# Performance work log

Hardware: AMD Instinct MI355X
Metric: run time of the kernel (lower is better)

Reference implementation:

```python
import jax, jax.numpy as jnp
import numpy as np

D = 1024
H = 16
HD = D // H
S = 1024
FF = 4 * D
EPS = 1e-5


def _layernorm(x, g, b):
    mu = jnp.mean(x, axis=-1, keepdims=True)
    var = jnp.var(x, axis=-1, keepdims=True)
    return (x - mu) * jax.lax.rsqrt(var + EPS) * g + b


def _mha(q_in, k_in, v_in, wq, bq, wk, bk, wv, bv, wo, bo, causal):
    # weights stored [in, out]; per-head torch Linears concatenated == one [D, D] projection
    def split(x, w, bias):
        y = x @ w + bias                      # [B, S, D]
        B, L, _ = y.shape
        return y.reshape(B, L, H, HD).transpose(0, 2, 1, 3)  # [B, H, L, HD]

    q = split(q_in, wq, bq)
    k = split(k_in, wk, bk)
    v = split(v_in, wv, bv)
    scores = jnp.einsum('bhqd,bhkd->bhqk', q, k) / np.sqrt(HD).astype(np.float32)
    if causal:
        mask = jnp.triu(jnp.ones((scores.shape[-2], scores.shape[-1]), dtype=bool), 1)
        scores = jnp.where(mask, -jnp.inf, scores)
    attn = jax.nn.softmax(scores, axis=-1)
    rep = jnp.einsum('bhqk,bhkd->bhqd', attn, v)
    B, _, L, _ = rep.shape
    rep = rep.transpose(0, 2, 1, 3).reshape(B, L, D)
    return rep @ wo + bo


def setup_inputs() -> dict:
    key = jax.random.key(0)
    ks = jax.random.split(key, 24)
    sc = 0.02
    d = {}
    d['decoder'] = jax.random.normal(ks[0], (8, S, D), dtype=jnp.float32)
    d['encoder'] = jax.random.normal(ks[1], (8, S, D), dtype=jnp.float32)
    names = ['sa_wq', 'sa_wk', 'sa_wv', 'sa_wo', 'ca_wq', 'ca_wk', 'ca_wv', 'ca_wo']
    for i, n in enumerate(names):
        d[n] = jax.random.normal(ks[2 + i], (D, D), dtype=jnp.float32) * sc
        d[n.replace('w', 'b')] = jnp.zeros((D,), dtype=jnp.float32)
    for i in range(1, 4):
        d[f'ln{i}_g'] = jnp.ones((D,), dtype=jnp.float32)
        d[f'ln{i}_b'] = jnp.zeros((D,), dtype=jnp.float32)
    d['ffn_w1'] = jax.random.normal(ks[10], (D, FF), dtype=jnp.float32) * sc
    d['ffn_b1'] = jnp.zeros((FF,), dtype=jnp.float32)
    d['ffn_w2'] = jax.random.normal(ks[11], (FF, D), dtype=jnp.float32) * sc
    d['ffn_b2'] = jnp.zeros((D,), dtype=jnp.float32)
    return d


def reference(decoder, encoder,
              sa_wq, sa_bq, sa_wk, sa_bk, sa_wv, sa_bv, sa_wo, sa_bo,
              ca_wq, ca_bq, ca_wk, ca_bk, ca_wv, ca_bv, ca_wo, ca_bo,
              ln1_g, ln1_b, ln2_g, ln2_b, ln3_g, ln3_b,
              ffn_w1, ffn_b1, ffn_w2, ffn_b2):
    # masked self-attention; NOTE: residual uses the *normalized* embeddings (faithful to source)
    x = _layernorm(decoder, ln1_g, ln1_b)
    x = x + _mha(x, x, x, sa_wq, sa_bq, sa_wk, sa_bk, sa_wv, sa_bv, sa_wo, sa_bo, causal=True)
    # cross-attention to (unnormalized) encoder output
    y = _layernorm(x, ln2_g, ln2_b)
    y = y + _mha(y, encoder, encoder, ca_wq, ca_bq, ca_wk, ca_bk, ca_wv, ca_bv, ca_wo, ca_bo, causal=False)
    # GELU FFN
    z = _layernorm(y, ln3_g, ln3_b)
    h = jax.nn.gelu(z @ ffn_w1 + ffn_b1, approximate=False)
    out = z + (h @ ffn_w2 + ffn_b2)
    return out
```

## Files before the change

kernel.cpp:

```cpp
#include <hip/hip_runtime.h>
#include <math.h>

typedef unsigned short u16;
typedef unsigned int u32;

typedef __attribute__((ext_vector_type(8))) short short8;
typedef __attribute__((ext_vector_type(4))) float floatx4;
typedef __attribute__((ext_vector_type(4))) unsigned short ushort4v;

#define DD 1024
#define HH 16
#define HD 64
#define SS 1024
#define BBATCH 8
#define FFDIM 4096
#define MM (BBATCH*SS)

__device__ __forceinline__ float bf2f(u16 v){ u32 x = ((u32)v)<<16; return __builtin_bit_cast(float, x); }
__device__ __forceinline__ u16 f2bf(float f){
  u32 x = __builtin_bit_cast(u32, f);
  u32 r = (x + 0x7fffu + ((x>>16)&1u)) >> 16;
  return (u16)r;
}

__device__ __forceinline__ void gload_lds16(const void* g, void* l){
  __builtin_amdgcn_global_load_lds((const __attribute__((address_space(1))) void*)g,
                                   (__attribute__((address_space(3))) void*)l, 16, 0, 0);
}

__global__ __launch_bounds__(256) void wtrans_k(const float* __restrict__ W,
                                                u16* __restrict__ Wt, int K, int N)
{
  __shared__ u16 tile[64][68];
  const int nt = blockIdx.x*64, kt = blockIdx.y*64;
  const int t = threadIdx.x;
  const int kl = t>>4, nl4 = (t&15)*4;
  #pragma unroll
  for (int r=0;r<4;r++){
    float4 v = *(const float4*)(W + (size_t)(kt + r*16 + kl)*N + nt + nl4);
    ushort4v u; u.x=f2bf(v.x); u.y=f2bf(v.y); u.z=f2bf(v.z); u.w=f2bf(v.w);
    *(ushort4v*)(&tile[r*16+kl][nl4]) = u;
  }
  __syncthreads();
  #pragma unroll
  for (int r=0;r<16;r++){
    int idx = r*256 + t;
    int nl = idx>>6, klc = idx&63;
    Wt[(size_t)(nt+nl)*K + kt + klc] = tile[klc][nl];
  }
}

__global__ __launch_bounds__(256) void cast_k(const float* __restrict__ in, u16* __restrict__ out)
{
  size_t i = (size_t)blockIdx.x*256 + threadIdx.x;
  #pragma unroll
  for (int r=0;r<4;r++){
    size_t idx = i + (size_t)r*524288;
    float4 v = ((const float4*)in)[idx];
    ushort4v u; u.x=f2bf(v.x); u.y=f2bf(v.y); u.z=f2bf(v.z); u.w=f2bf(v.w);
    ((ushort4v*)out)[idx] = u;
  }
}

template<int IN_BF16>
__global__ __launch_bounds__(256) void ln_k(const void* __restrict__ inv,
    const float* __restrict__ g, const float* __restrict__ bb, u16* __restrict__ out)
{
  const int row = blockIdx.x, t = threadIdx.x;
  float x[4];
  if (IN_BF16){
    const u16* in = (const u16*)inv;
    ushort4v v = ((const ushort4v*)(in + (size_t)row*DD))[t];
    #pragma unroll
    for (int i=0;i<4;i++) x[i]=bf2f(v[i]);
  } else {
    const float* in = (const float*)inv;
    float4 v = ((const float4*)(in + (size_t)row*DD))[t];
    x[0]=v.x; x[1]=v.y; x[2]=v.z; x[3]=v.w;
  }
  float s = x[0]+x[1]+x[2]+x[3];
  float q = x[0]*x[0]+x[1]*x[1]+x[2]*x[2]+x[3]*x[3];
  #pragma unroll
  for (int m=32;m;m>>=1){ s += __shfl_down(s,m); q += __shfl_down(q,m); }
  __shared__ float red[8];
  const int lane=t&63, wid=t>>6;
  if (lane==0){ red[wid]=s; red[wid+4]=q; }
  __syncthreads();
  s = red[0]+red[1]+red[2]+red[3];
  q = red[4]+red[5]+red[6]+red[7];
  const float mu = s*(1.0f/1024.0f);
  const float var = q*(1.0f/1024.0f) - mu*mu;
  const float rs = rsqrtf(var + 1e-5f);
  const int c = t*4;
  ushort4v ov;
  #pragma unroll
  for (int i=0;i<4;i++){
    float y = (x[i]-mu)*rs*g[c+i] + bb[c+i];
    ov[i] = f2bf(y);
  }
  ((ushort4v*)(out + (size_t)row*DD))[t] = ov;
}

template<int MODE>
__global__ __launch_bounds__(256) void gemm_k(
    const u16* __restrict__ A, const u16* __restrict__ Bt,
    const float* __restrict__ bias, const u16* __restrict__ res,
    void* __restrict__ Cout, int N, int K)
{
  __shared__ u16 smem[8192];
  u16* sA = smem; u16* sB = smem + 4096;
  const int t = threadIdx.x;
  const int gx = gridDim.x;
  int bid = blockIdx.y * gx + blockIdx.x;
  const int nwg = gx * gridDim.y;
  bid = (bid & 7) * (nwg >> 3) + (bid >> 3);
  const int n0 = (bid % gx) * 128, m0 = (bid / gx) * 128;
  const int lane = t & 63, wid = t >> 6;
  const int wr = wid >> 1, wc = wid & 1;
  const int lrow = lane & 15, lk8 = (lane >> 4) * 8;

  floatx4 acc[4][4];
  #pragma unroll
  for (int i=0;i<4;i++)
    #pragma unroll
    for (int j=0;j<4;j++) acc[i][j] = (floatx4)0.0f;

  const u16* gA = A + (size_t)m0 * K;
  const u16* gB = Bt + (size_t)n0 * K;
  const int c0row = t >> 2, c0col = (t & 3) * 8;
  const int nk = K >> 5;
  for (int kt = 0; kt < nk; ++kt) {
    const u16* gAk = gA + kt*32;
    const u16* gBk = gB + kt*32;
    gload_lds16(gAk + (size_t)c0row * K + c0col,      sA + t*8);
    gload_lds16(gAk + (size_t)(c0row+64) * K + c0col, sA + 2048 + t*8);
    gload_lds16(gBk + (size_t)c0row * K + c0col,      sB + t*8);
    gload_lds16(gBk + (size_t)(c0row+64) * K + c0col, sB + 2048 + t*8);
    __syncthreads();
    short8 a[4], b[4];
    #pragma unroll
    for (int mi=0; mi<4; mi++) a[mi] = *(const short8*)(sA + (wr*64 + mi*16 + lrow)*32 + lk8);
    #pragma unroll
    for (int ni=0; ni<4; ni++) b[ni] = *(const short8*)(sB + (wc*64 + ni*16 + lrow)*32 + lk8);
    #pragma unroll
    for (int mi=0; mi<4; mi++)
      #pragma unroll
      for (int ni=0; ni<4; ni++)
        acc[mi][ni] = __builtin_amdgcn_mfma_f32_16x16x32_bf16(a[mi], b[ni], acc[mi][ni], 0,0,0);
    __syncthreads();
  }

  #pragma unroll
  for (int mi=0; mi<4; mi++) {
    const int row_base = m0 + wr*64 + mi*16 + (lane>>4)*4;
    #pragma unroll
    for (int ni=0; ni<4; ni++) {
      const int col = n0 + wc*64 + ni*16 + lrow;
      const float bv = bias[col];
      floatx4 v = acc[mi][ni];
      #pragma unroll
      for (int r=0;r<4;r++){
        const int row = row_base + r;
        float x = v[r] + bv;
        const size_t f = (size_t)row * N + col;
        if (MODE==0){
          const int b = row >> 10, s = row & 1023;
          const int h = col >> 6, d = col & 63;
          ((u16*)Cout)[ (((size_t)(b*HH+h)*SS + s)<<6) + d ] = f2bf(x);
        } else if (MODE==1){
          ((u16*)Cout)[f] = f2bf(x + bf2f(res[f]));
        } else if (MODE==2){
          float gx2 = 0.5f * x * (1.0f + erff(x * 0.70710678f));
          ((u16*)Cout)[f] = f2bf(gx2);
        } else {
          ((float*)Cout)[f] = x + bf2f(res[f]);
        }
      }
    }
  }
}

template<int CAUSAL>
__global__ __launch_bounds__(256) void attn_k(
  const u16* __restrict__ Q, const u16* __restrict__ Kk, const u16* __restrict__ V,
  u16* __restrict__ rep)
{
  __shared__ u16 klds[64][72];
  __shared__ u16 vtf[4096];
  __shared__ u16 plds[4096];
  const int t = threadIdx.x, lane = t&63, wid = t>>6;
  int bidx = blockIdx.x;
  if (!CAUSAL) bidx = (bidx & 7) * 256 + (bidx >> 3);
  const int qb = bidx & 15;
  const int bh = bidx >> 4;
  const int q0 = qb*64;
  const int qw = q0 + wid*16;
  const int lrow = lane&15, hi = lane>>4, lk8 = hi*8;
  const int q8 = lrow & 7;
  const int qrow = qw + lrow;
  const size_t base = (size_t)bh * SS * HD;

  short8 qf[2];
  {
    const u16* qp = Q + base + (size_t)(qw + lrow)*HD + lk8;
    qf[0] = *(const short8*)(qp);
    qf[1] = *(const short8*)(qp + 32);
  }
  floatx4 o[4];
  #pragma unroll
  for (int co=0;co<4;co++) o[co] = (floatx4)0.0f;
  float mrow = -INFINITY, lsum = 0.f;

  const int ntiles = CAUSAL ? (qb + 1) : (SS >> 6);
  for (int kt=0; kt<ntiles; ++kt){
    const int k0 = kt<<6;
    short8 kreg[2], vreg[2];
    #pragma unroll
    for (int rr=0; rr<2; ++rr){
      const int idx = rr*256 + t;
      const int row = idx>>3, c8 = (idx&7)*8;
      kreg[rr] = *(const short8*)(Kk + base + (size_t)(k0+row)*HD + c8);
      vreg[rr] = *(const short8*)(V  + base + (size_t)(k0+row)*HD + c8);
    }
    __syncthreads();
    #pragma unroll
    for (int rr=0; rr<2; ++rr){
      const int idx = rr*256 + t;
      const int row = idx>>3, c8 = (idx&7)*8;
      *(short8*)(&klds[row][c8]) = kreg[rr];
      #pragma unroll
      for (int j=0;j<8;j++){
        const int d = c8+j;
        vtf[d*64 + ((((row>>3) ^ (d&7) ^ (d>>3))&7)<<3) + (row&7)] = (u16)vreg[rr][j];
      }
    }
    __syncthreads();

    float pr[4][4];
    #pragma unroll
    for (int co=0;co<4;co++){
      short8 kf0 = *(const short8*)(&klds[co*16+lrow][lk8]);
      short8 kf1 = *(const short8*)(&klds[co*16+lrow][32+lk8]);
      floatx4 z = (floatx4)0.0f;
      z = __builtin_amdgcn_mfma_f32_16x16x32_bf16(kf0, qf[0], z, 0,0,0);
      z = __builtin_amdgcn_mfma_f32_16x16x32_bf16(kf1, qf[1], z, 0,0,0);
      #pragma unroll
      for (int r=0;r<4;r++){
        float s = z[r]*0.125f;
        if (CAUSAL){
          const int key = k0 + co*16 + hi*4 + r;
          if (key > qrow) s = -INFINITY;
        }
        pr[co][r] = s;
      }
    }
    float tm = pr[0][0];
    #pragma unroll
    for (int co=0;co<4;co++)
      #pragma unroll
      for (int r=0;r<4;r++) tm = fmaxf(tm, pr[co][r]);
    tm = fmaxf(tm, __shfl_xor(tm, 16));
    tm = fmaxf(tm, __shfl_xor(tm, 32));
    const float mn = fmaxf(mrow, tm);
    const float al = __expf(mrow - mn);
    float ts = 0.f;
    #pragma unroll
    for (int co=0;co<4;co++)
      #pragma unroll
      for (int r=0;r<4;r++){
        const float p = __expf(pr[co][r]-mn);
        ts += p;
        const int klo = hi*4 + r;
        plds[wid*1024 + lrow*64 + ((((co*2 + (hi>>1)) ^ q8)&7)<<3) + (klo&7)] = f2bf(p);
      }
    ts += __shfl_xor(ts, 16);
    ts += __shfl_xor(ts, 32);
    lsum = lsum*al + ts;
    mrow = mn;
    #pragma unroll
    for (int co=0;co<4;co++) o[co] *= al;

    asm volatile("s_waitcnt lgkmcnt(0)" ::: "memory");
    __builtin_amdgcn_sched_barrier(0);
    short8 pf0 = *(const short8*)(plds + wid*1024 + lrow*64 + (((hi   ^ q8)&7)<<3));
    short8 pf1 = *(const short8*)(plds + wid*1024 + lrow*64 + ((((hi+4)^ q8)&7)<<3));
    #pragma unroll
    for (int co=0; co<4; co++){
      const int d = co*16 + lrow;
      const int sx = (d&7) ^ (d>>3);
      short8 vf0 = *(const short8*)(vtf + d*64 + (((hi   ^ sx)&7)<<3));
      short8 vf1 = *(const short8*)(vtf + d*64 + ((((hi+4)^ sx)&7)<<3));
      o[co] = __builtin_amdgcn_mfma_f32_16x16x32_bf16(vf0, pf0, o[co], 0,0,0);
      o[co] = __builtin_amdgcn_mfma_f32_16x16x32_bf16(vf1, pf1, o[co], 0,0,0);
    }
    __syncthreads();
  }

  const float rl = 1.0f / lsum;
  #pragma unroll
  for (int co=0;co<4;co++)
    #pragma unroll
    for (int r=0;r<4;r++){
      const int d = co*16 + hi*4 + r;
      plds[wid*1024 + lrow*64 + ((((d>>3) ^ q8)&7)<<3) + (d&7)] = f2bf(o[co][r]*rl);
    }
  asm volatile("s_waitcnt lgkmcnt(0)" ::: "memory");
  __builtin_amdgcn_sched_barrier(0);
  const int b = bh >> 4, h = bh & 15;
  #pragma unroll
  for (int it=0; it<2; ++it){
    const int idx = it*64 + lane;
    const int q = idx>>3, ch = idx&7;
    short8 vv = *(const short8*)(plds + wid*1024 + q*64 + (((ch ^ (q&7))&7)<<3));
    *(short8*)(rep + (((size_t)(b*SS + qw + q))<<10) + h*64 + ch*8) = vv;
  }
}

extern "C" void kernel_launch(void* const* d_in, const int* in_sizes, int n_in,
                              void* d_out, int out_size, void* d_ws, size_t ws_size,
                              hipStream_t stream) {
  const float* decoder = (const float*)d_in[0];
  const float* encoder = (const float*)d_in[1];
  const float* sa_wq = (const float*)d_in[2];  const float* sa_bq = (const float*)d_in[3];
  const float* sa_wk = (const float*)d_in[4];  const float* sa_bk = (const float*)d_in[5];
  const float* sa_wv = (const float*)d_in[6];  const float* sa_bv = (const float*)d_in[7];
  const float* sa_wo = (const float*)d_in[8];  const float* sa_bo = (const float*)d_in[9];
  const float* ca_wq = (const float*)d_in[10]; const float* ca_bq = (const float*)d_in[11];
  const float* ca_wk = (const float*)d_in[12]; const float* ca_bk = (const float*)d_in[13];
  const float* ca_wv = (const float*)d_in[14]; const float* ca_bv = (const float*)d_in[15];
  const float* ca_wo = (const float*)d_in[16]; const float* ca_bo = (const float*)d_in[17];
  const float* ln1_g = (const float*)d_in[18]; const float* ln1_b = (const float*)d_in[19];
  const float* ln2_g = (const float*)d_in[20]; const float* ln2_b = (const float*)d_in[21];
  const float* ln3_g = (const float*)d_in[22]; const float* ln3_b = (const float*)d_in[23];
  const float* ffn_w1 = (const float*)d_in[24]; const float* ffn_b1 = (const float*)d_in[25];
  const float* ffn_w2 = (const float*)d_in[26]; const float* ffn_b2 = (const float*)d_in[27];

  char* ws = (char*)d_ws;
  const size_t MB = 1u<<20;
  u16* wt_saq = (u16*)(ws + 0*MB);
  u16* wt_sak = (u16*)(ws + 2*MB);
  u16* wt_sav = (u16*)(ws + 4*MB);
  u16* wt_sao = (u16*)(ws + 6*MB);
  u16* wt_caq = (u16*)(ws + 8*MB);
  u16* wt_cak = (u16*)(ws + 10*MB);
  u16* wt_cav = (u16*)(ws + 12*MB);
  u16* wt_cao = (u16*)(ws + 14*MB);
  u16* wt_w1  = (u16*)(ws + 16*MB);
  u16* wt_w2  = (u16*)(ws + 24*MB);
  u16* enc_bf = (u16*)(ws + 32*MB);
  u16* lnbuf  = (u16*)(ws + 48*MB);
  u16* qbuf   = (u16*)(ws + 64*MB);
  u16* kbuf   = (u16*)(ws + 80*MB);
  u16* vbuf   = (u16*)(ws + 96*MB);
  u16* repbuf = (u16*)(ws + 112*MB);
  u16* x2buf  = (u16*)(ws + 128*MB);
  u16* hbuf   = (u16*)(ws + 144*MB);

  const dim3 blk(256);
  wtrans_k<<<dim3(16,16), blk, 0, stream>>>(sa_wq, wt_saq, DD, DD);
  wtrans_k<<<dim3(16,16), blk, 0, stream>>>(sa_wk, wt_sak, DD, DD);
  wtrans_k<<<dim3(16,16), blk, 0, stream>>>(sa_wv, wt_sav, DD, DD);
  wtrans_k<<<dim3(16,16), blk, 0, stream>>>(sa_wo, wt_sao, DD, DD);
  wtrans_k<<<dim3(16,16), blk, 0, stream>>>(ca_wq, wt_caq, DD, DD);
  wtrans_k<<<dim3(16,16), blk, 0, stream>>>(ca_wk, wt_cak, DD, DD);
  wtrans_k<<<dim3(16,16), blk, 0, stream>>>(ca_wv, wt_cav, DD, DD);
  wtrans_k<<<dim3(16,16), blk, 0, stream>>>(ca_wo, wt_cao, DD, DD);
  wtrans_k<<<dim3(64,16), blk, 0, stream>>>(ffn_w1, wt_w1, DD, FFDIM);
  wtrans_k<<<dim3(16,64), blk, 0, stream>>>(ffn_w2, wt_w2, FFDIM, DD);
  cast_k<<<dim3(2048), blk, 0, stream>>>(encoder, enc_bf);
  ln_k<0><<<dim3(MM), blk, 0, stream>>>(decoder, ln1_g, ln1_b, lnbuf);
  gemm_k<0><<<dim3(8,64), blk, 0, stream>>>(lnbuf, wt_saq, sa_bq, nullptr, qbuf, DD, DD);
  gemm_k<0><<<dim3(8,64), blk, 0, stream>>>(lnbuf, wt_sak, sa_bk, nullptr, kbuf, DD, DD);
  gemm_k<0><<<dim3(8,64), blk, 0, stream>>>(lnbuf, wt_sav, sa_bv, nullptr, vbuf, DD, DD);
  attn_k<1><<<dim3(2048), blk, 0, stream>>>(qbuf, kbuf, vbuf, repbuf);
  gemm_k<1><<<dim3(8,64), blk, 0, stream>>>(repbuf, wt_sao, sa_bo, lnbuf, x2buf, DD, DD);
  ln_k<1><<<dim3(MM), blk, 0, stream>>>(x2buf, ln2_g, ln2_b, lnbuf);
  gemm_k<0><<<dim3(8,64), blk, 0, stream>>>(lnbuf,  wt_caq, ca_bq, nullptr, qbuf, DD, DD);
  gemm_k<0><<<dim3(8,64), blk, 0, stream>>>(enc_bf, wt_cak, ca_bk, nullptr, kbuf, DD, DD);
  gemm_k<0><<<dim3(8,64), blk, 0, stream>>>(enc_bf, wt_cav, ca_bv, nullptr, vbuf, DD, DD);
  attn_k<0><<<dim3(2048), blk, 0, stream>>>(qbuf, kbuf, vbuf, repbuf);
  gemm_k<1><<<dim3(8,64), blk, 0, stream>>>(repbuf, wt_cao, ca_bo, lnbuf, x2buf, DD, DD);
  ln_k<1><<<dim3(MM), blk, 0, stream>>>(x2buf, ln3_g, ln3_b, lnbuf);
  gemm_k<2><<<dim3(32,64), blk, 0, stream>>>(lnbuf, wt_w1, ffn_b1, nullptr, hbuf, FFDIM, DD);
  gemm_k<3><<<dim3(8,64), blk, 0, stream>>>(hbuf, wt_w2, ffn_b2, lnbuf, d_out, DD, FFDIM);
}
```

Before: 883.6 us.

## Use 256x256 eight-wave pipelined GEMM with fused QKV and split-K FFN2

```diff
diff --git a/kernel.cpp b/kernel.cpp
--- a/kernel.cpp
+++ b/kernel.cpp
@@ -101,62 +101,111 @@
   ((ushort4v*)(out + (size_t)row*DD))[t] = ov;
 }
 
+#define FRAG_A(mi, ks) (*(const short8*)(At  + (wm*128 + (mi)*16 + lrow)*64 + ((((ks)*4+hi) ^ swz)*8)))
+#define FRAG_B(ni, ks) (*(const short8*)(Btl + (wn*64  + (ni)*16 + lrow)*64 + ((((ks)*4+hi) ^ swz)*8)))
+
+#define GPHASE(BUF, PP, STAGECALL, DOVM)                                      \
+  { const u16* At  = &lds[(BUF)*32768];                                       \
+    const u16* Btl = &lds[(BUF)*32768 + 16384];                               \
+    if ((PP)==0){                                                             \
+      _Pragma("unroll") for (int ni=0; ni<4; ni++){                           \
+        bfr[ni][0] = FRAG_B(ni, 0);                                           \
+        bfr[ni][1] = FRAG_B(ni, 1);                                           \
+      }                                                                       \
+    }                                                                         \
+    short8 af0k0 = FRAG_A((PP)*2+0, 0), af0k1 = FRAG_A((PP)*2+0, 1);          \
+    short8 af1k0 = FRAG_A((PP)*2+1, 0), af1k1 = FRAG_A((PP)*2+1, 1);          \
+    STAGECALL;                                                                \
+    if (DOVM) { asm volatile("s_waitcnt vmcnt(4)" ::: "memory"); }            \
+    __builtin_amdgcn_s_barrier();                                             \
+    __builtin_amdgcn_sched_barrier(0);                                        \
+    __builtin_amdgcn_s_setprio(1);                                            \
+    _Pragma("unroll") for (int ni=0; ni<4; ni++){                             \
+      acc[(PP)*2+0][ni] = __builtin_amdgcn_mfma_f32_16x16x32_bf16(af0k0, bfr[ni][0], acc[(PP)*2+0][ni], 0,0,0); \
+      acc[(PP)*2+0][ni] = __builtin_amdgcn_mfma_f32_16x16x32_bf16(af0k1, bfr[ni][1], acc[(PP)*2+0][ni], 0,0,0); \
+      acc[(PP)*2+1][ni] = __builtin_amdgcn_mfma_f32_16x16x32_bf16(af1k0, bfr[ni][0], acc[(PP)*2+1][ni], 0,0,0); \
+      acc[(PP)*2+1][ni] = __builtin_amdgcn_mfma_f32_16x16x32_bf16(af1k1, bfr[ni][1], acc[(PP)*2+1][ni], 0,0,0); \
+    }                                                                         \
+    __builtin_amdgcn_s_setprio(0);                                            \
+    __builtin_amdgcn_sched_barrier(0);                                        \
+    __builtin_amdgcn_s_barrier();                                             \
+    __builtin_amdgcn_sched_barrier(0);                                        \
+  }
+
 template<int MODE>
-__global__ __launch_bounds__(256) void gemm_k(
+__global__ __launch_bounds__(512, 2) void gemm8_k(
     const u16* __restrict__ A, const u16* __restrict__ Bt,
-    const float* __restrict__ bias, const u16* __restrict__ res,
-    void* __restrict__ Cout, int N, int K)
-{
-  __shared__ u16 smem[8192];
-  u16* sA = smem; u16* sB = smem + 4096;
+    const float* __restrict__ b0, const float* __restrict__ b1, const float* __restrict__ b2,
+    const u16* __restrict__ res, void* __restrict__ Cout,
+    int N, int K, int nk, int nbx)
+{
+  __shared__ __align__(16) u16 lds[65536];
   const int t = threadIdx.x;
-  const int gx = gridDim.x;
-  int bid = blockIdx.y * gx + blockIdx.x;
-  const int nwg = gx * gridDim.y;
+  int bid = blockIdx.x;
+  const int nwg = gridDim.x;
   bid = (bid & 7) * (nwg >> 3) + (bid >> 3);
-  const int n0 = (bid % gx) * 128, m0 = (bid / gx) * 128;
+  int koff = 0; size_t outoff = 0;
+  if (MODE==4){ const int half = bid >> 7; bid &= 127; koff = half*2048; outoff = (size_t)half*8388608; }
+  const int n0 = (bid % nbx) * 256;
+  const int m0 = (bid / nbx) * 256;
   const int lane = t & 63, wid = t >> 6;
-  const int wr = wid >> 1, wc = wid & 1;
-  const int lrow = lane & 15, lk8 = (lane >> 4) * 8;
-
-  floatx4 acc[4][4];
-  #pragma unroll
-  for (int i=0;i<4;i++)
+  const int wm = wid >> 2, wn = wid & 3;
+  const int lrow = lane & 15, hi = lane >> 4;
+  const int swz = lrow & 7;
+
+  floatx4 acc[8][4];
+  #pragma unroll
+  for (int i=0;i<8;i++)
     #pragma unroll
     for (int j=0;j<4;j++) acc[i][j] = (floatx4)0.0f;
-
-  const u16* gA = A + (size_t)m0 * K;
-  const u16* gB = Bt + (size_t)n0 * K;
-  const int c0row = t >> 2, c0col = (t & 3) * 8;
-  const int nk = K >> 5;
-  for (int kt = 0; kt < nk; ++kt) {
-    const u16* gAk = gA + kt*32;
-    const u16* gBk = gB + kt*32;
-    gload_lds16(gAk + (size_t)c0row * K + c0col,      sA + t*8);
-    gload_lds16(gAk + (size_t)(c0row+64) * K + c0col, sA + 2048 + t*8);
-    gload_lds16(gBk + (size_t)c0row * K + c0col,      sB + t*8);
-    gload_lds16(gBk + (size_t)(c0row+64) * K + c0col, sB + 2048 + t*8);
-    __syncthreads();
-    short8 a[4], b[4];
-    #pragma unroll
-    for (int mi=0; mi<4; mi++) a[mi] = *(const short8*)(sA + (wr*64 + mi*16 + lrow)*32 + lk8);
-    #pragma unroll
-    for (int ni=0; ni<4; ni++) b[ni] = *(const short8*)(sB + (wc*64 + ni*16 + lrow)*32 + lk8);
-    #pragma unroll
-    for (int mi=0; mi<4; mi++)
-      #pragma unroll
-      for (int ni=0; ni<4; ni++)
-        acc[mi][ni] = __builtin_amdgcn_mfma_f32_16x16x32_bf16(a[mi], b[ni], acc[mi][ni], 0,0,0);
-    __syncthreads();
-  }
-
-  #pragma unroll
-  for (int mi=0; mi<4; mi++) {
-    const int row_base = m0 + wr*64 + mi*16 + (lane>>4)*4;
+  short8 bfr[4][2];
+
+  const u16* gA0 = A  + (size_t)m0       * K + koff;
+  const u16* gA1 = A  + (size_t)(m0+128) * K + koff;
+  const u16* gB0 = Bt + (size_t)n0       * K + koff;
+  const u16* gB1 = Bt + (size_t)(n0+128) * K + koff;
+
+  const int sr = t >> 3;
+  const int sg = ((t & 7) ^ (sr & 7)) * 8;
+  auto stage = [&](const u16* gbase, int kt, int ldsoff){
+    const u16* g = gbase + (size_t)sr*K + kt*64 + sg;
+    gload_lds16(g,                 &lds[ldsoff + t*8]);
+    gload_lds16(g + (size_t)64*K,  &lds[ldsoff + 4096 + t*8]);
+  };
+
+  stage(gA0, 0, 0);      stage(gA1, 0, 8192);
+  stage(gB0, 0, 16384);  stage(gB1, 0, 24576);
+  stage(gB0, 1, 49152);  stage(gB1, 1, 57344);
+  asm volatile("s_waitcnt vmcnt(4)" ::: "memory");
+  __builtin_amdgcn_s_barrier();
+  __builtin_amdgcn_sched_barrier(0);
+
+  const int mask = nk - 1;
+  for (int j = 0; j < (nk >> 1); ++j){
+    const int c0 = 2*j;
+    const int k1 = c0 + 1;
+    const int k2 = (c0 + 2) & mask;
+    const int k3 = (c0 + 3) & mask;
+    GPHASE(0, 0, stage(gA0, k1, 32768), 0)
+    GPHASE(0, 1, stage(gA1, k1, 40960), 0)
+    GPHASE(0, 2, stage(gB0, k2, 16384), 0)
+    GPHASE(0, 3, stage(gB1, k2, 24576), 1)
+    GPHASE(1, 0, stage(gA0, k2, 0),     0)
+    GPHASE(1, 1, stage(gA1, k2, 8192),  0)
+    GPHASE(1, 2, stage(gB0, k3, 49152), 0)
+    GPHASE(1, 3, stage(gB1, k3, 57344), 1)
+  }
+  asm volatile("s_waitcnt vmcnt(0)" ::: "memory");
+
+  #pragma unroll
+  for (int mi=0; mi<8; mi++) {
+    const int row_base = m0 + wm*128 + mi*16 + hi*4;
     #pragma unroll
     for (int ni=0; ni<4; ni++) {
-      const int col = n0 + wc*64 + ni*16 + lrow;
-      const float bv = bias[col];
+      const int col = n0 + wn*64 + ni*16 + lrow;
+      float bv = 0.f;
+      if (MODE==0){ const float* bp = (col<1024)?b0:((col<2048)?b1:b2); bv = bp[col&1023]; }
+      else if (MODE==1 || MODE==2) bv = b0[col];
       floatx4 v = acc[mi][ni];
       #pragma unroll
       for (int r=0;r<4;r++){
@@ -164,20 +213,39 @@
         float x = v[r] + bv;
         const size_t f = (size_t)row * N + col;
         if (MODE==0){
-          const int b = row >> 10, s = row & 1023;
-          const int h = col >> 6, d = col & 63;
-          ((u16*)Cout)[ (((size_t)(b*HH+h)*SS + s)<<6) + d ] = f2bf(x);
+          const int bb = row >> 10, s = row & 1023;
+          const int cc = col & 1023;
+          const int h = cc >> 6, d = cc & 63;
+          ((u16*)Cout)[ (size_t)(col>>10)*8388608 + (((size_t)(bb*HH+h)*SS + s)<<6) + d ] = f2bf(x);
         } else if (MODE==1){
           ((u16*)Cout)[f] = f2bf(x + bf2f(res[f]));
         } else if (MODE==2){
           float gx2 = 0.5f * x * (1.0f + erff(x * 0.70710678f));
           ((u16*)Cout)[f] = f2bf(gx2);
         } else {
-          ((float*)Cout)[f] = x + bf2f(res[f]);
+          ((float*)Cout)[outoff + f] = x;
         }
       }
     }
   }
+}
+
+__global__ __launch_bounds__(256) void combine_k(
+    const float* __restrict__ p0, const float* __restrict__ p1,
+    const float* __restrict__ bias, const u16* __restrict__ res, float* __restrict__ out)
+{
+  const size_t i = (size_t)blockIdx.x*256 + threadIdx.x;
+  float4 a = ((const float4*)p0)[i];
+  float4 b = ((const float4*)p1)[i];
+  const int col = ((int)(i & 255)) * 4;
+  float4 bv = *(const float4*)(bias + col);
+  ushort4v r = ((const ushort4v*)res)[i];
+  float4 o;
+  o.x = a.x + b.x + bv.x + bf2f(r.x);
+  o.y = a.y + b.y + bv.y + bf2f(r.y);
+  o.z = a.z + b.z + bv.z + bf2f(r.z);
+  o.w = a.w + b.w + bv.w + bf2f(r.w);
+  ((float4*)out)[i] = o;
 }
 
 template<int CAUSAL>
@@ -355,6 +423,7 @@
   u16* repbuf = (u16*)(ws + 112*MB);
   u16* x2buf  = (u16*)(ws + 128*MB);
   u16* hbuf   = (u16*)(ws + 144*MB);
+  float* pbuf = (float*)(ws + 64*MB);
 
   const dim3 blk(256);
   wtrans_k<<<dim3(16,16), blk, 0, stream>>>(sa_wq, wt_saq, DD, DD);
@@ -369,18 +438,23 @@
   wtrans_k<<<dim3(16,64), blk, 0, stream>>>(ffn_w2, wt_w2, FFDIM, DD);
   cast_k<<<dim3(2048), blk, 0, stream>>>(encoder, enc_bf);
   ln_k<0><<<dim3(MM), blk, 0, stream>>>(decoder, ln1_g, ln1_b, lnbuf);
-  gemm_k<0><<<dim3(8,64), blk, 0, stream>>>(lnbuf, wt_saq, sa_bq, nullptr, qbuf, DD, DD);
-  gemm_k<0><<<dim3(8,64), blk, 0, stream>>>(lnbuf, wt_sak, sa_bk, nullptr, kbuf, DD, DD);
-  gemm_k<0><<<dim3(8,64), blk, 0, stream>>>(lnbuf, wt_sav, sa_bv, nullptr, vbuf, DD, DD);
+  gemm8_k<0><<<dim3(384), dim3(512), 0, stream>>>(lnbuf, wt_saq, sa_bq, sa_bk, sa_bv,
+      nullptr, qbuf, 3072, 1024, 16, 12);
   attn_k<1><<<dim3(2048), blk, 0, stream>>>(qbuf, kbuf, vbuf, repbuf);
-  gemm_k<1><<<dim3(8,64), blk, 0, stream>>>(repbuf, wt_sao, sa_bo, lnbuf, x2buf, DD, DD);
+  gemm8_k<1><<<dim3(128), dim3(512), 0, stream>>>(repbuf, wt_sao, sa_bo, nullptr, nullptr,
+      lnbuf, x2buf, 1024, 1024, 16, 4);
   ln_k<1><<<dim3(MM), blk, 0, stream>>>(x2buf, ln2_g, ln2_b, lnbuf);
-  gemm_k<0><<<dim3(8,64), blk, 0, stream>>>(lnbuf,  wt_caq, ca_bq, nullptr, qbuf, DD, DD);
-  gemm_k<0><<<dim3(8,64), blk, 0, stream>>>(enc_bf, wt_cak, ca_bk, nullptr, kbuf, DD, DD);
-  gemm_k<0><<<dim3(8,64), blk, 0, stream>>>(enc_bf, wt_cav, ca_bv, nullptr, vbuf, DD, DD);
+  gemm8_k<0><<<dim3(128), dim3(512), 0, stream>>>(lnbuf, wt_caq, ca_bq, nullptr, nullptr,
+      nullptr, qbuf, 1024, 1024, 16, 4);
+  gemm8_k<0><<<dim3(256), dim3(512), 0, stream>>>(enc_bf, wt_cak, ca_bk, ca_bv, nullptr,
+      nullptr, kbuf, 2048, 1024, 16, 8);
   attn_k<0><<<dim3(2048), blk, 0, stream>>>(qbuf, kbuf, vbuf, repbuf);
-  gemm_k<1><<<dim3(8,64), blk, 0, stream>>>(repbuf, wt_cao, ca_bo, lnbuf, x2buf, DD, DD);
+  gemm8_k<1><<<dim3(128), dim3(512), 0, stream>>>(repbuf, wt_cao, ca_bo, nullptr, nullptr,
+      lnbuf, x2buf, 1024, 1024, 16, 4);
   ln_k<1><<<dim3(MM), blk, 0, stream>>>(x2buf, ln3_g, ln3_b, lnbuf);
-  gemm_k<2><<<dim3(32,64), blk, 0, stream>>>(lnbuf, wt_w1, ffn_b1, nullptr, hbuf, FFDIM, DD);
-  gemm_k<3><<<dim3(8,64), blk, 0, stream>>>(hbuf, wt_w2, ffn_b2, lnbuf, d_out, DD, FFDIM);
-}
+  gemm8_k<2><<<dim3(512), dim3(512), 0, stream>>>(lnbuf, wt_w1, ffn_b1, nullptr, nullptr,
+      nullptr, hbuf, 4096, 1024, 16, 16);
+  gemm8_k<4><<<dim3(256), dim3(512), 0, stream>>>(hbuf, wt_w2, nullptr, nullptr, nullptr,
+      nullptr, pbuf, 1024, 4096, 32, 4);
+  combine_k<<<dim3(8192), blk, 0, stream>>>(pbuf, pbuf + 8388608, ffn_b2, lnbuf, (float*)d_out);
+}
```

New measurement: 804.1 us. 1.1x faster.
